# Kernel tuning notes

Hardware: AMD Instinct MI355X
Metric: run time of the kernel (lower is better)

Reference implementation:

```python
import jax, jax.numpy as jnp
import numpy as np

N = 100000      # nodes
D = 128         # num_hidden_channels == num_output_feats
H = 4           # attention heads
HD = D // H     # head dim = 32
KNN = 20        # in-edges per node
E = N * KNN
BN_EPS = 1e-5


def setup_inputs() -> dict:
    key = jax.random.key(0)
    ks = jax.random.split(key, 20)
    s = 1.0 / np.sqrt(D)
    f = jax.random.normal(ks[0], (N, D), jnp.float32)
    src = jax.random.randint(ks[1], (E,), 0, N, dtype=jnp.int32)
    dst = jnp.repeat(jnp.arange(N, dtype=jnp.int32), KNN)  # knn in-edges per node
    return {
        "f": f,
        "src": src,
        "dst": dst,
        "bn1_gamma": jax.random.normal(ks[2], (D,), jnp.float32) * 0.1 + 1.0,
        "bn1_beta": jax.random.normal(ks[3], (D,), jnp.float32) * 0.1,
        "bn1_mean": jax.random.normal(ks[4], (D,), jnp.float32) * 0.1,
        "bn1_var": jax.random.uniform(ks[5], (D,), jnp.float32, 0.5, 1.5),
        "Wq": jax.random.normal(ks[6], (D, D), jnp.float32) * s,
        "Wk": jax.random.normal(ks[7], (D, D), jnp.float32) * s,
        "Wv": jax.random.normal(ks[8], (D, D), jnp.float32) * s,
        "Wo": jax.random.normal(ks[9], (D, D), jnp.float32) * s,
        "bo": jax.random.normal(ks[10], (D,), jnp.float32) * 0.01,
        "bn2_gamma": jax.random.normal(ks[11], (D,), jnp.float32) * 0.1 + 1.0,
        "bn2_beta": jax.random.normal(ks[12], (D,), jnp.float32) * 0.1,
        "bn2_mean": jax.random.normal(ks[13], (D,), jnp.float32) * 0.1,
        "bn2_var": jax.random.uniform(ks[14], (D,), jnp.float32, 0.5, 1.5),
        "W1": jax.random.normal(ks[15], (D, 2 * D), jnp.float32) * s,
        "W2": jax.random.normal(ks[16], (2 * D, D), jnp.float32) * (1.0 / np.sqrt(2 * D)),
    }


def _bn(x, gamma, beta, mean, var):
    # eval-mode BatchNorm1d with running statistics
    return (x - mean) * (gamma / jnp.sqrt(var + BN_EPS)) + beta


def reference(f, src, dst, bn1_gamma, bn1_beta, bn1_mean, bn1_var,
              Wq, Wk, Wv, Wo, bo,
              bn2_gamma, bn2_beta, bn2_mean, bn2_var, W1, W2):
    n = f.shape[0]
    h = _bn(f, bn1_gamma, bn1_beta, bn1_mean, bn1_var)
    q = (h @ Wq).reshape(n, H, HD)
    k = (h @ Wk).reshape(n, H, HD)
    v = (h @ Wv).reshape(n, H, HD)
    # edge-wise score: K[src] . Q[dst]  -> [E, H]
    score = jnp.einsum('ehd,ehd->eh', k[src], q[dst]) / np.sqrt(HD)
    score = jnp.exp(jnp.clip(score, -5.0, 5.0))
    # scatter-sum weighted V and normalizer to destination nodes
    wV = jax.ops.segment_sum(v[src] * score[:, :, None], dst, num_segments=n)  # [N,H,HD]
    z = jax.ops.segment_sum(score, dst, num_segments=n)                        # [N,H]
    attn = (wV / (z[:, :, None] + 1e-6)).reshape(n, D)
    node = attn @ Wo + bo
    node = f + node  # residual 1 (dropout is identity in eval)
    h2 = _bn(node, bn2_gamma, bn2_beta, bn2_mean, bn2_var)
    mlp = jax.nn.silu(h2 @ W1) @ W2
    return node + mlp  # residual 2
```

## Files before the change

kernel.cpp:

```cpp
#include <hip/hip_runtime.h>
#include <hip/hip_bf16.h>

#define NN 100000
#define DD 128
#define KNN 20

typedef unsigned short u16;
typedef __attribute__((ext_vector_type(8))) __bf16 bf16x8;
typedef __attribute__((ext_vector_type(4))) float f32x4;
typedef __attribute__((ext_vector_type(4))) unsigned short u16x4;
typedef __attribute__((ext_vector_type(8))) unsigned short u16x8;

__device__ __forceinline__ float b2f(u16 b) {
  unsigned int u = ((unsigned int)b) << 16;
  float f;
  __builtin_memcpy(&f, &u, 4);
  return f;
}
__device__ __forceinline__ u16 f2b(float f) {
  unsigned int u;
  __builtin_memcpy(&u, &f, 4);
  u += 0x7fffu + ((u >> 16) & 1u);
  return (u16)(u >> 16);
}

__global__ __launch_bounds__(256) void bn1_kernel(
    const float* __restrict__ f, const float* __restrict__ g, const float* __restrict__ be,
    const float* __restrict__ mu, const float* __restrict__ va, u16* __restrict__ h)
{
  int idx = (blockIdx.x * 256 + threadIdx.x) * 8;
  if (idx >= NN * DD) return;
  int c = idx & (DD - 1);
  u16x8 out;
#pragma unroll
  for (int j = 0; j < 8; j++) {
    float scale = g[c + j] * rsqrtf(va[c + j] + 1e-5f);
    out[j] = f2b((f[idx + j] - mu[c + j]) * scale + be[c + j]);
  }
  *(u16x8*)(h + idx) = out;
}

__device__ __forceinline__ void stage_frag(const float* __restrict__ W, int wstride,
                                           int colbase, u16* __restrict__ dst, int f, int KS) {
  int lane = f & 63;
  int t2 = f >> 6;
  int ks = t2 % KS;
  int ct = t2 / KS;
  int quad = lane >> 4, l16 = lane & 15;
  const float* src = W + (size_t)(ks * 32 + quad * 8) * wstride + colbase + ct * 16 + l16;
  u16x8 o;
#pragma unroll
  for (int j = 0; j < 8; j++) o[j] = f2b(src[(size_t)j * wstride]);
  *(u16x8*)(dst + (size_t)f * 8) = o;
}

__global__ __launch_bounds__(256) void stage_weights_kernel(
    const float* __restrict__ Wq, const float* __restrict__ Wk, const float* __restrict__ Wv,
    const float* __restrict__ Wo, const float* __restrict__ W1, const float* __restrict__ W2,
    u16* __restrict__ WTf)
{
  int t = blockIdx.x * 256 + threadIdx.x;
  if (t < 2048)       stage_frag(Wq, 128, 0,   WTf + 0,     t,         4);
  else if (t < 4096)  stage_frag(Wk, 128, 0,   WTf + 16384, t - 2048,  4);
  else if (t < 6144)  stage_frag(Wv, 128, 0,   WTf + 32768, t - 4096,  4);
  else if (t < 8192)  stage_frag(Wo, 128, 0,   WTf + 49152, t - 6144,  4);
  else if (t < 10240) stage_frag(W1, 256, 0,   WTf + 65536, t - 8192,  4);
  else if (t < 12288) stage_frag(W1, 256, 128, WTf + 81920, t - 10240, 4);
  else if (t < 16384) stage_frag(W2, 128, 0,   WTf + 98304, t - 12288, 8);
}

template <int K, int NB, int MODE>
__global__ __launch_bounds__(256) void gemm2_kernel(
    const u16* __restrict__ A, const u16* __restrict__ Bf,
    u16* __restrict__ o0, u16* __restrict__ o1, u16* __restrict__ o2,
    float* __restrict__ of, float* __restrict__ nodef,
    const float* __restrict__ fres, const float* __restrict__ bo,
    const float* __restrict__ g2, const float* __restrict__ b2,
    const float* __restrict__ m2, const float* __restrict__ v2,
    const float* __restrict__ nodein, int nrows)
{
  constexpr int KS = K / 32;
  const int wave = threadIdx.x >> 6;
  const int lane = threadIdx.x & 63;
  const int quad = lane >> 4;
  const int l16 = lane & 15;
  const int rowbase = blockIdx.x * 128 + wave * 32;

  bf16x8 a[2][KS];
#pragma unroll
  for (int rt = 0; rt < 2; rt++) {
    int arow = rowbase + rt * 16 + l16;
    if (arow >= nrows) arow = nrows - 1;
    const u16* Ap = A + (size_t)arow * K + quad * 8;
#pragma unroll
    for (int ks = 0; ks < KS; ks++) a[rt][ks] = *(const bf16x8*)(Ap + ks * 32);
  }

#pragma unroll
  for (int m = 0; m < NB; m++) {
    const u16* Bm = Bf + (size_t)m * (128 * K);
    f32x4 acc[2][8];
#pragma unroll
    for (int rt = 0; rt < 2; rt++)
#pragma unroll
      for (int ct = 0; ct < 8; ct++) acc[rt][ct] = (f32x4){0.f, 0.f, 0.f, 0.f};

#pragma unroll
    for (int ct = 0; ct < 8; ct++) {
#pragma unroll
      for (int ks = 0; ks < KS; ks++) {
        bf16x8 b = *(const bf16x8*)(Bm + (size_t)((ct * KS + ks) * 64 + lane) * 8);
        acc[0][ct] = __builtin_amdgcn_mfma_f32_16x16x32_bf16(a[0][ks], b, acc[0][ct], 0, 0, 0);
        acc[1][ct] = __builtin_amdgcn_mfma_f32_16x16x32_bf16(a[1][ks], b, acc[1][ct], 0, 0, 0);
      }
    }

#pragma unroll
    for (int rt = 0; rt < 2; rt++) {
#pragma unroll
      for (int ct = 0; ct < 8; ct++) {
        int coll = ct * 16 + l16;
#pragma unroll
        for (int r = 0; r < 4; r++) {
          int row = rowbase + rt * 16 + quad * 4 + r;
          if (row >= nrows) continue;
          float val = acc[rt][ct][r];
          if (MODE == 0) {
            u16* dst = (m == 0) ? o0 : (m == 1) ? o1 : o2;
            dst[(size_t)row * DD + coll] = f2b(val);
          } else if (MODE == 1) {
            float nv = val + bo[coll] + fres[(size_t)row * DD + coll];
            nodef[(size_t)row * DD + coll] = nv;
            float sc2 = g2[coll] * rsqrtf(v2[coll] + 1e-5f);
            o0[(size_t)row * DD + coll] = f2b((nv - m2[coll]) * sc2 + b2[coll]);
          } else if (MODE == 2) {
            int col = m * 128 + coll;
            float s = val / (1.f + __expf(-val));
            o0[(size_t)row * 256 + col] = f2b(s);
          } else {
            of[(size_t)row * DD + coll] = val + nodein[(size_t)row * DD + coll];
          }
        }
      }
    }
  }
}

__global__ __launch_bounds__(256) void attn_kernel(
    const u16* __restrict__ q, const u16* __restrict__ k, const u16* __restrict__ v,
    const int* __restrict__ src, u16* __restrict__ attn)
{
  const int node = blockIdx.x * 8 + (threadIdx.x >> 5);
  const int sub = threadIdx.x & 31;
  const int c0 = sub * 4;
  const size_t base = (size_t)node * DD + c0;

  u16x4 qr = *(const u16x4*)(q + base);
  const float qv0 = b2f(qr[0]), qv1 = b2f(qr[1]), qv2 = b2f(qr[2]), qv3 = b2f(qr[3]);

  int sv[KNN];
  const int* sp = src + (size_t)node * KNN;
#pragma unroll
  for (int j = 0; j < KNN; j++) sv[j] = sp[j];

  float a0 = 0.f, a1 = 0.f, a2 = 0.f, a3 = 0.f, z = 0.f;
  const float inv_sqrt_hd = 0.17677669529663687f;
#pragma unroll 5
  for (int j = 0; j < KNN; j++) {
    const size_t eb = (size_t)sv[j] * DD + c0;
    u16x4 kr = *(const u16x4*)(k + eb);
    u16x4 vr = *(const u16x4*)(v + eb);
    float p = b2f(kr[0]) * qv0 + b2f(kr[1]) * qv1 + b2f(kr[2]) * qv2 + b2f(kr[3]) * qv3;
    p += __shfl_xor(p, 1);
    p += __shfl_xor(p, 2);
    p += __shfl_xor(p, 4);
    float sc = __expf(fminf(fmaxf(p * inv_sqrt_hd, -5.f), 5.f));
    z += sc;
    a0 += sc * b2f(vr[0]);
    a1 += sc * b2f(vr[1]);
    a2 += sc * b2f(vr[2]);
    a3 += sc * b2f(vr[3]);
  }
  float inv = 1.f / (z + 1e-6f);
  u16x4 o;
  o[0] = f2b(a0 * inv); o[1] = f2b(a1 * inv);
  o[2] = f2b(a2 * inv); o[3] = f2b(a3 * inv);
  *(u16x4*)(attn + base) = o;
}

extern "C" void kernel_launch(void* const* d_in, const int* in_sizes, int n_in,
                              void* d_out, int out_size, void* d_ws, size_t ws_size,
                              hipStream_t stream) {
  const float* f  = (const float*)d_in[0];
  const int* src  = (const int*)d_in[1];
  const float* g1 = (const float*)d_in[3];
  const float* b1 = (const float*)d_in[4];
  const float* m1 = (const float*)d_in[5];
  const float* v1 = (const float*)d_in[6];
  const float* Wq = (const float*)d_in[7];
  const float* Wk = (const float*)d_in[8];
  const float* Wv = (const float*)d_in[9];
  const float* Wo = (const float*)d_in[10];
  const float* bo = (const float*)d_in[11];
  const float* g2 = (const float*)d_in[12];
  const float* b2 = (const float*)d_in[13];
  const float* m2 = (const float*)d_in[14];
  const float* v2 = (const float*)d_in[15];
  const float* W1 = (const float*)d_in[16];
  const float* W2 = (const float*)d_in[17];
  float* out = (float*)d_out;

  char* ws = (char*)d_ws;
  const size_t SZ = (size_t)NN * DD * 2;
  u16*  h     = (u16*)(ws + 0);
  u16*  qb    = (u16*)(ws + SZ);
  u16*  kb    = (u16*)(ws + 2 * SZ);
  u16*  vb    = (u16*)(ws + 3 * SZ);
  float* node = (float*)(ws + 4 * SZ);
  u16*  inter = (u16*)(ws + 2 * SZ);
  u16*  attn  = h;
  u16*  h2    = qb;
  u16*  WTf   = (u16*)(ws + 6 * SZ);

  const int g2grid = (NN + 127) / 128;

  bn1_kernel<<<(NN * DD / 8 + 255) / 256, 256, 0, stream>>>(f, g1, b1, m1, v1, h);
  stage_weights_kernel<<<64, 256, 0, stream>>>(Wq, Wk, Wv, Wo, W1, W2, WTf);

  gemm2_kernel<128, 3, 0><<<g2grid, 256, 0, stream>>>(
      h, WTf + 0, qb, kb, vb, nullptr, nullptr,
      nullptr, nullptr, nullptr, nullptr, nullptr, nullptr, nullptr, NN);

  attn_kernel<<<NN / 8, 256, 0, stream>>>(qb, kb, vb, src, attn);

  gemm2_kernel<128, 1, 1><<<g2grid, 256, 0, stream>>>(
      attn, WTf + 49152, h2, nullptr, nullptr, nullptr, node,
      f, bo, g2, b2, m2, v2, nullptr, NN);

  gemm2_kernel<128, 2, 2><<<g2grid, 256, 0, stream>>>(
      h2, WTf + 65536, inter, nullptr, nullptr, nullptr, nullptr,
      nullptr, nullptr, nullptr, nullptr, nullptr, nullptr, nullptr, NN);

  gemm2_kernel<256, 1, 3><<<g2grid, 256, 0, stream>>>(
      inter, WTf + 98304, nullptr, nullptr, nullptr, out, nullptr,
      nullptr, nullptr, nullptr, nullptr, nullptr, nullptr, node, NN);
}
```

Before: 472.5 us.

## Interleave K and V into one buffer and stage GEMM weights through LDS

New measurement: 533.8 us. 1.13x slower.

```diff
diff --git a/kernel.cpp b/kernel.cpp
--- a/kernel.cpp
+++ b/kernel.cpp
@@ -41,11 +41,13 @@
 }
 
 __device__ __forceinline__ void stage_frag(const float* __restrict__ W, int wstride,
-                                           int colbase, u16* __restrict__ dst, int f, int KS) {
+                                           int colbase, u16* __restrict__ dst, int f) {
   int lane = f & 63;
   int t2 = f >> 6;
-  int ks = t2 % KS;
-  int ct = t2 / KS;
+  int ksl = t2 & 3;
+  int ct = (t2 >> 2) & 7;
+  int kc = t2 >> 5;
+  int ks = kc * 4 + ksl;
   int quad = lane >> 4, l16 = lane & 15;
   const float* src = W + (size_t)(ks * 32 + quad * 8) * wstride + colbase + ct * 16 + l16;
   u16x8 o;
@@ -60,19 +62,19 @@
     u16* __restrict__ WTf)
 {
   int t = blockIdx.x * 256 + threadIdx.x;
-  if (t < 2048)       stage_frag(Wq, 128, 0,   WTf + 0,     t,         4);
-  else if (t < 4096)  stage_frag(Wk, 128, 0,   WTf + 16384, t - 2048,  4);
-  else if (t < 6144)  stage_frag(Wv, 128, 0,   WTf + 32768, t - 4096,  4);
-  else if (t < 8192)  stage_frag(Wo, 128, 0,   WTf + 49152, t - 6144,  4);
-  else if (t < 10240) stage_frag(W1, 256, 0,   WTf + 65536, t - 8192,  4);
-  else if (t < 12288) stage_frag(W1, 256, 128, WTf + 81920, t - 10240, 4);
-  else if (t < 16384) stage_frag(W2, 128, 0,   WTf + 98304, t - 12288, 8);
+  if (t < 2048)       stage_frag(Wq, 128, 0,   WTf + 0,     t);
+  else if (t < 4096)  stage_frag(Wk, 128, 0,   WTf + 16384, t - 2048);
+  else if (t < 6144)  stage_frag(Wv, 128, 0,   WTf + 32768, t - 4096);
+  else if (t < 8192)  stage_frag(Wo, 128, 0,   WTf + 49152, t - 6144);
+  else if (t < 10240) stage_frag(W1, 256, 0,   WTf + 65536, t - 8192);
+  else if (t < 12288) stage_frag(W1, 256, 128, WTf + 81920, t - 10240);
+  else if (t < 16384) stage_frag(W2, 128, 0,   WTf + 98304, t - 12288);
 }
 
 template <int K, int NB, int MODE>
-__global__ __launch_bounds__(256) void gemm2_kernel(
+__global__ __launch_bounds__(256) void gemm3_kernel(
     const u16* __restrict__ A, const u16* __restrict__ Bf,
-    u16* __restrict__ o0, u16* __restrict__ o1, u16* __restrict__ o2,
+    u16* __restrict__ o0, u16* __restrict__ o1,
     float* __restrict__ of, float* __restrict__ nodef,
     const float* __restrict__ fres, const float* __restrict__ bo,
     const float* __restrict__ g2, const float* __restrict__ b2,
@@ -80,8 +82,11 @@
     const float* __restrict__ nodein, int nrows)
 {
   constexpr int KS = K / 32;
-  const int wave = threadIdx.x >> 6;
-  const int lane = threadIdx.x & 63;
+  constexpr int NC = K / 128;
+  __shared__ u16 Bs[16384];
+  const int tid = threadIdx.x;
+  const int wave = tid >> 6;
+  const int lane = tid & 63;
   const int quad = lane >> 4;
   const int l16 = lane & 15;
   const int rowbase = blockIdx.x * 128 + wave * 32;
@@ -106,12 +111,21 @@
       for (int ct = 0; ct < 8; ct++) acc[rt][ct] = (f32x4){0.f, 0.f, 0.f, 0.f};
 
 #pragma unroll
-    for (int ct = 0; ct < 8; ct++) {
-#pragma unroll
-      for (int ks = 0; ks < KS; ks++) {
-        bf16x8 b = *(const bf16x8*)(Bm + (size_t)((ct * KS + ks) * 64 + lane) * 8);
-        acc[0][ct] = __builtin_amdgcn_mfma_f32_16x16x32_bf16(a[0][ks], b, acc[0][ct], 0, 0, 0);
-        acc[1][ct] = __builtin_amdgcn_mfma_f32_16x16x32_bf16(a[1][ks], b, acc[1][ct], 0, 0, 0);
+    for (int kc = 0; kc < NC; kc++) {
+      __syncthreads();
+      const u16* srcp = Bm + kc * 16384 + tid * 8;
+#pragma unroll
+      for (int i = 0; i < 8; i++)
+        *(u16x8*)(Bs + i * 2048 + tid * 8) = *(const u16x8*)(srcp + i * 2048);
+      __syncthreads();
+#pragma unroll
+      for (int ct = 0; ct < 8; ct++) {
+#pragma unroll
+        for (int ksl = 0; ksl < 4; ksl++) {
+          bf16x8 b = *(const bf16x8*)(Bs + ((ct * 4 + ksl) * 64 + lane) * 8);
+          acc[0][ct] = __builtin_amdgcn_mfma_f32_16x16x32_bf16(a[0][kc * 4 + ksl], b, acc[0][ct], 0, 0, 0);
+          acc[1][ct] = __builtin_amdgcn_mfma_f32_16x16x32_bf16(a[1][kc * 4 + ksl], b, acc[1][ct], 0, 0, 0);
+        }
       }
     }
 
@@ -126,8 +140,9 @@
           if (row >= nrows) continue;
           float val = acc[rt][ct][r];
           if (MODE == 0) {
-            u16* dst = (m == 0) ? o0 : (m == 1) ? o1 : o2;
-            dst[(size_t)row * DD + coll] = f2b(val);
+            if (m == 0) o0[(size_t)row * DD + coll] = f2b(val);
+            else if (m == 1) o1[(size_t)row * 256 + coll * 2] = f2b(val);
+            else o1[(size_t)row * 256 + coll * 2 + 1] = f2b(val);
           } else if (MODE == 1) {
             float nv = val + bo[coll] + fres[(size_t)row * DD + coll];
             nodef[(size_t)row * DD + coll] = nv;
@@ -147,15 +162,15 @@
 }
 
 __global__ __launch_bounds__(256) void attn_kernel(
-    const u16* __restrict__ q, const u16* __restrict__ k, const u16* __restrict__ v,
+    const u16* __restrict__ q, const u16* __restrict__ kv,
     const int* __restrict__ src, u16* __restrict__ attn)
 {
   const int node = blockIdx.x * 8 + (threadIdx.x >> 5);
   const int sub = threadIdx.x & 31;
   const int c0 = sub * 4;
-  const size_t base = (size_t)node * DD + c0;
-
-  u16x4 qr = *(const u16x4*)(q + base);
+  const size_t qbase = (size_t)node * DD + c0;
+
+  u16x4 qr = *(const u16x4*)(q + qbase);
   const float qv0 = b2f(qr[0]), qv1 = b2f(qr[1]), qv2 = b2f(qr[2]), qv3 = b2f(qr[3]);
 
   int sv[KNN];
@@ -165,27 +180,25 @@
 
   float a0 = 0.f, a1 = 0.f, a2 = 0.f, a3 = 0.f, z = 0.f;
   const float inv_sqrt_hd = 0.17677669529663687f;
-#pragma unroll 5
+#pragma unroll
   for (int j = 0; j < KNN; j++) {
-    const size_t eb = (size_t)sv[j] * DD + c0;
-    u16x4 kr = *(const u16x4*)(k + eb);
-    u16x4 vr = *(const u16x4*)(v + eb);
-    float p = b2f(kr[0]) * qv0 + b2f(kr[1]) * qv1 + b2f(kr[2]) * qv2 + b2f(kr[3]) * qv3;
+    u16x8 kvr = *(const u16x8*)(kv + (size_t)sv[j] * 256 + c0 * 2);
+    float p = b2f(kvr[0]) * qv0 + b2f(kvr[2]) * qv1 + b2f(kvr[4]) * qv2 + b2f(kvr[6]) * qv3;
     p += __shfl_xor(p, 1);
     p += __shfl_xor(p, 2);
     p += __shfl_xor(p, 4);
     float sc = __expf(fminf(fmaxf(p * inv_sqrt_hd, -5.f), 5.f));
     z += sc;
-    a0 += sc * b2f(vr[0]);
-    a1 += sc * b2f(vr[1]);
-    a2 += sc * b2f(vr[2]);
-    a3 += sc * b2f(vr[3]);
+    a0 += sc * b2f(kvr[1]);
+    a1 += sc * b2f(kvr[3]);
+    a2 += sc * b2f(kvr[5]);
+    a3 += sc * b2f(kvr[7]);
   }
   float inv = 1.f / (z + 1e-6f);
   u16x4 o;
   o[0] = f2b(a0 * inv); o[1] = f2b(a1 * inv);
   o[2] = f2b(a2 * inv); o[3] = f2b(a3 * inv);
-  *(u16x4*)(attn + base) = o;
+  *(u16x4*)(attn + qbase) = o;
 }
 
 extern "C" void kernel_launch(void* const* d_in, const int* in_sizes, int n_in,
@@ -214,34 +227,33 @@
   const size_t SZ = (size_t)NN * DD * 2;
   u16*  h     = (u16*)(ws + 0);
   u16*  qb    = (u16*)(ws + SZ);
-  u16*  kb    = (u16*)(ws + 2 * SZ);
-  u16*  vb    = (u16*)(ws + 3 * SZ);
+  u16*  kv    = (u16*)(ws + 2 * SZ);
   float* node = (float*)(ws + 4 * SZ);
   u16*  inter = (u16*)(ws + 2 * SZ);
   u16*  attn  = h;
   u16*  h2    = qb;
   u16*  WTf   = (u16*)(ws + 6 * SZ);
 
-  const int g2grid = (NN + 127) / 128;
+  const int g3grid = (NN + 127) / 128;
 
   bn1_kernel<<<(NN * DD / 8 + 255) / 256, 256, 0, stream>>>(f, g1, b1, m1, v1, h);
   stage_weights_kernel<<<64, 256, 0, stream>>>(Wq, Wk, Wv, Wo, W1, W2, WTf);
 
-  gemm2_kernel<128, 3, 0><<<g2grid, 256, 0, stream>>>(
-      h, WTf + 0, qb, kb, vb, nullptr, nullptr,
+  gemm3_kernel<128, 3, 0><<<g3grid, 256, 0, stream>>>(
+      h, WTf + 0, qb, kv, nullptr, nullptr,
       nullptr, nullptr, nullptr, nullptr, nullptr, nullptr, nullptr, NN);
 
-  attn_kernel<<<NN / 8, 256, 0, stream>>>(qb, kb, vb, src, attn);
-
-  gemm2_kernel<128, 1, 1><<<g2grid, 256, 0, stream>>>(
-      attn, WTf + 49152, h2, nullptr, nullptr, nullptr, node,
+  attn_kernel<<<NN / 8, 256, 0, stream>>>(qb, kv, src, attn);
+
+  gemm3_kernel<128, 1, 1><<<g3grid, 256, 0, stream>>>(
+      attn, WTf + 49152, h2, nullptr, nullptr, node,
       f, bo, g2, b2, m2, v2, nullptr, NN);
 
-  gemm2_kernel<128, 2, 2><<<g2grid, 256, 0, stream>>>(
-      h2, WTf + 65536, inter, nullptr, nullptr, nullptr, nullptr,
+  gemm3_kernel<128, 2, 2><<<g3grid, 256, 0, stream>>>(
+      h2, WTf + 65536, inter, nullptr, nullptr, nullptr,
       nullptr, nullptr, nullptr, nullptr, nullptr, nullptr, nullptr, NN);
 
-  gemm2_kernel<256, 1, 3><<<g2grid, 256, 0, stream>>>(
-      inter, WTf + 98304, nullptr, nullptr, nullptr, out, nullptr,
+  gemm3_kernel<256, 1, 3><<<g3grid, 256, 0, stream>>>(
+      inter, WTf + 98304, nullptr, nullptr, out, nullptr,
       nullptr, nullptr, nullptr, nullptr, nullptr, nullptr, node, NN);
 }
```
